# Performance work log

Measured on AMD Instinct MI355X. Metric: run time of the kernel, lower is better.

## Reference

```python
import jax, jax.numpy as jnp
import numpy as np

B, C, H, W = 16, 256, 32, 32
NUM_LAYERS = 30
OUT = 16  # sqrt(out_channels)
EPS = 1e-5


def setup_inputs() -> dict:
    key = jax.random.key(0)
    k1, k2, k3 = jax.random.split(key, 3)
    x = jax.random.normal(k1, (B, C, H, W), dtype=jnp.float32)
    # delta_t ~ small positive values (module inits ~N(0.01, 0.005))
    delta_t = jax.random.uniform(k2, (NUM_LAYERS, 1), dtype=jnp.float32) * 0.02
    matrices = jax.random.normal(k3, (NUM_LAYERS, 1, 1, OUT, OUT), dtype=jnp.float32) * 0.1
    gamma = jnp.ones((H * W,), dtype=jnp.float32)   # BatchNorm2d weight, oc = i*i = H*W
    beta = jnp.zeros((H * W,), dtype=jnp.float32)   # BatchNorm2d bias
    return {"x": x, "delta_t": delta_t, "matrices": matrices, "gamma": gamma, "beta": beta}


def _bn_relu6(z, gamma, beta):
    # training-mode BatchNorm2d over channel axis 1 (channels = H*W), then ReLU6
    mean = jnp.mean(z, axis=(0, 2, 3), keepdims=True)
    var = jnp.mean(jnp.square(z - mean), axis=(0, 2, 3), keepdims=True)  # biased var
    zhat = (z - mean) * jax.lax.rsqrt(var + EPS)
    g = gamma.reshape(1, -1, 1, 1)
    b = beta.reshape(1, -1, 1, 1)
    return jnp.clip(zhat * g + b, 0.0, 6.0)


def reference(x, delta_t, matrices, gamma, beta):
    b, c, h, w = x.shape
    hw = h * w
    # feature_reshape: [B,C,H,W] -> [B,HW,C] -> [B,HW,out,out] (inn == out branch)
    x1 = x.reshape(b, c, hw).transpose(0, 2, 1).reshape(b, hw, OUT, OUT)
    dt = jnp.clip(delta_t, 0.0, 6.0)[:, 0]  # relu6(delta_t), shape [L]

    def step(y0, params):
        m, dtl = params  # m: [1,1,out,out] broadcasts elementwise against x1
        dydt = -y0 + _bn_relu6(y0 + m * x1, gamma, beta)
        return y0 + dtl * dydt, None

    y0, _ = jax.lax.scan(step, x1, (matrices, dt))
    # (y0 + x1): [B, HW, out, out] -> view [B,H,W,out*out] -> permute to [B,out*out,H,W]
    y = (y0 + x1).reshape(b, h, w, OUT * OUT).transpose(0, 3, 1, 2)
    return y
```

## Files before the change

kernel.cpp:

```cpp
#include <hip/hip_runtime.h>

typedef float v2f __attribute__((ext_vector_type(2)));

#define HW      1024
#define NLAYERS 30
#define TPB     256

template <int CTRL, int RMASK>
__device__ __forceinline__ float dpp_add(float x) {
    int t = __builtin_amdgcn_update_dpp(0, __builtin_bit_cast(int, x),
                                        CTRL, RMASK, 0xf, true);
    return x + __builtin_bit_cast(float, t);
}
__device__ __forceinline__ float wave_sum64(float x) {
    x = dpp_add<0x111, 0xf>(x);
    x = dpp_add<0x112, 0xf>(x);
    x = dpp_add<0x114, 0xf>(x);
    x = dpp_add<0x118, 0xf>(x);
    x = dpp_add<0x142, 0xa>(x);
    x = dpp_add<0x143, 0xc>(x);
    return x;
}

__global__ __launch_bounds__(TPB) void ode_fused(const float* __restrict__ x,
                                                 const float* __restrict__ delta_t,
                                                 const float* __restrict__ matrices,
                                                 const float* __restrict__ gamma,
                                                 const float* __restrict__ beta,
                                                 float* __restrict__ out) {
    const int bid = blockIdx.x;
    const int p   = ((bid & 7) << 7) | (bid >> 3);
    const int t   = threadIdx.x;

    __shared__ float smat[(NLAYERS + 1) * 256];
    __shared__ float sdt[NLAYERS];
    __shared__ __align__(16) v2f red[2][4];

#pragma unroll
    for (int i = 0; i < NLAYERS; ++i)
        smat[i * 256 + t] = matrices[i * 256 + t];
    if (t < NLAYERS)
        sdt[t] = __builtin_amdgcn_fmed3f(delta_t[t], 0.0f, 6.0f);

    v2f x1[8], y[8];
#pragma unroll
    for (int k = 0; k < 8; ++k) {
        x1[k].x = x[(size_t)(t + 512 * k) * HW + p];
        x1[k].y = x[(size_t)(t + 512 * k + 256) * HW + p];
        y[k] = x1[k];
    }

    const float gp   = gamma[p];
    const float bp   = beta[p];
    const int   wid  = t >> 6;
    const int   lane = t & 63;

    __syncthreads();
    float m_cur = smat[t];

    for (int l = 0; l < NLAYERS; ++l) {
        const float dtl = sdt[l];
        const v2f m2    = {m_cur, m_cur};
        const v2f dt2   = {dtl, dtl};
        const v2f om2   = {1.0f - dtl, 1.0f - dtl};

        v2f z[8];
        v2f sA = {0.f, 0.f}, sB = {0.f, 0.f};
        v2f qA = {0.f, 0.f}, qB = {0.f, 0.f};
#pragma unroll
        for (int k = 0; k < 8; k += 2) {
            z[k]     = __builtin_elementwise_fma(m2, x1[k], y[k]);
            z[k + 1] = __builtin_elementwise_fma(m2, x1[k + 1], y[k + 1]);
            sA += z[k];
            sB += z[k + 1];
            qA = __builtin_elementwise_fma(z[k], z[k], qA);
            qB = __builtin_elementwise_fma(z[k + 1], z[k + 1], qB);
        }
#pragma unroll
        for (int k = 0; k < 8; ++k) y[k] *= om2;

        const v2f sv = sA + sB;
        const v2f qv = qA + qB;
        float s = wave_sum64(sv.x + sv.y);
        float q = wave_sum64(qv.x + qv.y);

        const int par = l & 1;
        if (lane == 63) { v2f w; w.x = s; w.y = q; red[par][wid] = w; }
        m_cur = smat[(l + 1) * 256 + t];
        __syncthreads();

        const float4 r0 = *(const float4*)&red[par][0];
        const float4 r1 = *(const float4*)&red[par][2];
        const float S  = (r0.x + r0.z) + (r1.x + r1.z);
        const float S2 = (r0.y + r0.w) + (r1.y + r1.w);

        const float mean = S * (1.0f / 4096.0f);
        const float var  = fmaf(-mean, mean, S2 * (1.0f / 4096.0f));
        const float rstd = rsqrtf(var + 1e-5f);
        const float g    = gp * rstd;
        const float bb   = fmaf(-mean, g, bp);
        const v2f g2 = {g, g}, b2 = {bb, bb};
        const v2f z0 = {0.f, 0.f}, s6 = {6.f, 6.f};
#pragma unroll
        for (int k = 0; k < 8; ++k) {
            v2f a = __builtin_elementwise_fma(z[k], g2, b2);
            a = __builtin_elementwise_max(a, z0);
            a = __builtin_elementwise_min(a, s6);
            y[k] = __builtin_elementwise_fma(dt2, a, y[k]);
        }
    }

#pragma unroll
    for (int k = 0; k < 8; ++k) {
        out[(size_t)(t + 512 * k) * HW + p]       = y[k].x + x1[k].x;
        out[(size_t)(t + 512 * k + 256) * HW + p] = y[k].y + x1[k].y;
    }
}

extern "C" void kernel_launch(void* const* d_in, const int* in_sizes, int n_in,
                              void* d_out, int out_size, void* d_ws, size_t ws_size,
                              hipStream_t stream) {
    const float* x        = (const float*)d_in[0];
    const float* delta_t  = (const float*)d_in[1];
    const float* matrices = (const float*)d_in[2];
    const float* gamma    = (const float*)d_in[3];
    const float* beta     = (const float*)d_in[4];
    float* out = (float*)d_out;

    ode_fused<<<dim3(HW), dim3(TPB), 0, stream>>>(x, delta_t, matrices, gamma, beta, out);
}
```

Baseline: 116.0 us.

## Process each BN channel with a single wavefront to eliminate block barriers

```diff
diff --git a/kernel.cpp b/kernel.cpp
--- a/kernel.cpp
+++ b/kernel.cpp
@@ -4,7 +4,7 @@
 
 #define HW      1024
 #define NLAYERS 30
-#define TPB     256
+#define TPB     64
 
 template <int CTRL, int RMASK>
 __device__ __forceinline__ float dpp_add(float x) {
@@ -22,98 +22,98 @@
     return x;
 }
 
-__global__ __launch_bounds__(TPB) void ode_fused(const float* __restrict__ x,
-                                                 const float* __restrict__ delta_t,
-                                                 const float* __restrict__ matrices,
-                                                 const float* __restrict__ gamma,
-                                                 const float* __restrict__ beta,
-                                                 float* __restrict__ out) {
-    const int bid = blockIdx.x;
-    const int p   = ((bid & 7) << 7) | (bid >> 3);
-    const int t   = threadIdx.x;
+__global__ __launch_bounds__(TPB, 1) void ode_wave(
+    const float* __restrict__ x, const float* __restrict__ delta_t,
+    const float* __restrict__ matrices, const float* __restrict__ gamma,
+    const float* __restrict__ beta, float* __restrict__ out) {
 
-    __shared__ float smat[(NLAYERS + 1) * 256];
-    __shared__ float sdt[NLAYERS];
-    __shared__ __align__(16) v2f red[2][4];
+    const int bid  = blockIdx.x;
+    const int p    = ((bid & 7) << 7) | (bid >> 3);
+    const int lane = threadIdx.x;
 
+    v2f x1[4][8], y[4][8], z[4][8];
 #pragma unroll
-    for (int i = 0; i < NLAYERS; ++i)
-        smat[i * 256 + t] = matrices[i * 256 + t];
-    if (t < NLAYERS)
-        sdt[t] = __builtin_amdgcn_fmed3f(delta_t[t], 0.0f, 6.0f);
-
-    v2f x1[8], y[8];
+    for (int j = 0; j < 4; ++j) {
+        const size_t base = (size_t)(lane + 64 * j) * HW + p;
 #pragma unroll
-    for (int k = 0; k < 8; ++k) {
-        x1[k].x = x[(size_t)(t + 512 * k) * HW + p];
-        x1[k].y = x[(size_t)(t + 512 * k + 256) * HW + p];
-        y[k] = x1[k];
+        for (int i = 0; i < 8; ++i) {
+            x1[j][i].x = x[base + (size_t)(2 * i)     * 256 * HW];
+            x1[j][i].y = x[base + (size_t)(2 * i + 1) * 256 * HW];
+            y[j][i] = x1[j][i];
+        }
     }
 
-    const float gp   = gamma[p];
-    const float bp   = beta[p];
-    const int   wid  = t >> 6;
-    const int   lane = t & 63;
+    const float gp = gamma[p];
+    const float bp = beta[p];
 
-    __syncthreads();
-    float m_cur = smat[t];
+    float mn[4];
+#pragma unroll
+    for (int j = 0; j < 4; ++j) mn[j] = matrices[64 * j + lane];
+    float dtn = delta_t[0];
 
-    for (int l = 0; l < NLAYERS; ++l) {
-        const float dtl = sdt[l];
-        const v2f m2    = {m_cur, m_cur};
-        const v2f dt2   = {dtl, dtl};
-        const v2f om2   = {1.0f - dtl, 1.0f - dtl};
+    for (int lay = 0; lay < NLAYERS; ++lay) {
+        const float dt = __builtin_amdgcn_fmed3f(dtn, 0.0f, 6.0f);
+        v2f M[4];
+#pragma unroll
+        for (int j = 0; j < 4; ++j) { M[j].x = mn[j]; M[j].y = mn[j]; }
 
-        v2f z[8];
-        v2f sA = {0.f, 0.f}, sB = {0.f, 0.f};
-        v2f qA = {0.f, 0.f}, qB = {0.f, 0.f};
+        const int nl = (lay < NLAYERS - 1) ? lay + 1 : lay;
 #pragma unroll
-        for (int k = 0; k < 8; k += 2) {
-            z[k]     = __builtin_elementwise_fma(m2, x1[k], y[k]);
-            z[k + 1] = __builtin_elementwise_fma(m2, x1[k + 1], y[k + 1]);
-            sA += z[k];
-            sB += z[k + 1];
-            qA = __builtin_elementwise_fma(z[k], z[k], qA);
-            qB = __builtin_elementwise_fma(z[k + 1], z[k + 1], qB);
+        for (int j = 0; j < 4; ++j) mn[j] = matrices[nl * 256 + 64 * j + lane];
+        dtn = delta_t[nl];
+
+        v2f s[4], q[4];
+#pragma unroll
+        for (int j = 0; j < 4; ++j) {
+            s[j] = (v2f){0.0f, 0.0f};
+            q[j] = (v2f){0.0f, 0.0f};
         }
 #pragma unroll
-        for (int k = 0; k < 8; ++k) y[k] *= om2;
+        for (int j = 0; j < 4; ++j) {
+#pragma unroll
+            for (int i = 0; i < 8; ++i) {
+                const v2f zz = __builtin_elementwise_fma(M[j], x1[j][i], y[j][i]);
+                z[j][i] = zz;
+                s[j] += zz;
+                q[j] = __builtin_elementwise_fma(zz, zz, q[j]);
+            }
+        }
 
-        const v2f sv = sA + sB;
-        const v2f qv = qA + qB;
-        float s = wave_sum64(sv.x + sv.y);
-        float q = wave_sum64(qv.x + qv.y);
-
-        const int par = l & 1;
-        if (lane == 63) { v2f w; w.x = s; w.y = q; red[par][wid] = w; }
-        m_cur = smat[(l + 1) * 256 + t];
-        __syncthreads();
-
-        const float4 r0 = *(const float4*)&red[par][0];
-        const float4 r1 = *(const float4*)&red[par][2];
-        const float S  = (r0.x + r0.z) + (r1.x + r1.z);
-        const float S2 = (r0.y + r0.w) + (r1.y + r1.w);
+        const v2f sv = (s[0] + s[1]) + (s[2] + s[3]);
+        const v2f qv = (q[0] + q[1]) + (q[2] + q[3]);
+        const float ssum = wave_sum64(sv.x + sv.y);
+        const float qsum = wave_sum64(qv.x + qv.y);
+        const float S = __shfl(ssum, 63, 64);
+        const float Q = __shfl(qsum, 63, 64);
 
         const float mean = S * (1.0f / 4096.0f);
-        const float var  = fmaf(-mean, mean, S2 * (1.0f / 4096.0f));
+        const float var  = fmaf(-mean, mean, Q * (1.0f / 4096.0f));
         const float rstd = rsqrtf(var + 1e-5f);
         const float g    = gp * rstd;
         const float bb   = fmaf(-mean, g, bp);
-        const v2f g2 = {g, g}, b2 = {bb, bb};
-        const v2f z0 = {0.f, 0.f}, s6 = {6.f, 6.f};
+        const v2f g2 = {g, g}, b2 = {bb, bb}, dt2 = {dt, dt};
+
 #pragma unroll
-        for (int k = 0; k < 8; ++k) {
-            v2f a = __builtin_elementwise_fma(z[k], g2, b2);
-            a = __builtin_elementwise_max(a, z0);
-            a = __builtin_elementwise_min(a, s6);
-            y[k] = __builtin_elementwise_fma(dt2, a, y[k]);
+        for (int j = 0; j < 4; ++j) {
+#pragma unroll
+            for (int i = 0; i < 8; ++i) {
+                v2f a = __builtin_elementwise_fma(z[j][i], g2, b2);
+                a.x = __builtin_amdgcn_fmed3f(a.x, 0.0f, 6.0f);
+                a.y = __builtin_amdgcn_fmed3f(a.y, 0.0f, 6.0f);
+                const v2f d = a - y[j][i];
+                y[j][i] = __builtin_elementwise_fma(dt2, d, y[j][i]);
+            }
         }
     }
 
 #pragma unroll
-    for (int k = 0; k < 8; ++k) {
-        out[(size_t)(t + 512 * k) * HW + p]       = y[k].x + x1[k].x;
-        out[(size_t)(t + 512 * k + 256) * HW + p] = y[k].y + x1[k].y;
+    for (int j = 0; j < 4; ++j) {
+        const size_t base = (size_t)(lane + 64 * j) * HW + p;
+#pragma unroll
+        for (int i = 0; i < 8; ++i) {
+            out[base + (size_t)(2 * i)     * 256 * HW] = y[j][i].x + x1[j][i].x;
+            out[base + (size_t)(2 * i + 1) * 256 * HW] = y[j][i].y + x1[j][i].y;
+        }
     }
 }
 
@@ -127,5 +127,5 @@
     const float* beta     = (const float*)d_in[4];
     float* out = (float*)d_out;
 
-    ode_fused<<<dim3(HW), dim3(TPB), 0, stream>>>(x, delta_t, matrices, gamma, beta, out);
+    ode_wave<<<dim3(HW), dim3(TPB), 0, stream>>>(x, delta_t, matrices, gamma, beta, out);
 }
```

Measured after the change: 136.7 us. 1.18x slower.

## Transpose input to row-major workspace and run ODE on contiguous rows

Applied to the files above, without the earlier changes.

```diff
diff --git a/kernel.cpp b/kernel.cpp
--- a/kernel.cpp
+++ b/kernel.cpp
@@ -1,10 +1,25 @@
 #include <hip/hip_runtime.h>
 
 typedef float v2f __attribute__((ext_vector_type(2)));
+typedef float v4f __attribute__((ext_vector_type(4)));
 
 #define HW      1024
+#define NROWS   4096
 #define NLAYERS 30
 #define TPB     256
+
+static __device__ __forceinline__ v2f pk_fma(v2f a, v2f b, v2f c) {
+    v2f d; asm("v_pk_fma_f32 %0, %1, %2, %3" : "=v"(d) : "v"(a), "v"(b), "v"(c));
+    return d;
+}
+static __device__ __forceinline__ v2f pk_add(v2f a, v2f b) {
+    v2f d; asm("v_pk_add_f32 %0, %1, %2" : "=v"(d) : "v"(a), "v"(b));
+    return d;
+}
+static __device__ __forceinline__ v2f pk_mul(v2f a, v2f b) {
+    v2f d; asm("v_pk_mul_f32 %0, %1, %2" : "=v"(d) : "v"(a), "v"(b));
+    return d;
+}
 
 template <int CTRL, int RMASK>
 __device__ __forceinline__ float dpp_add(float x) {
@@ -20,6 +35,156 @@
     x = dpp_add<0x142, 0xa>(x);
     x = dpp_add<0x143, 0xc>(x);
     return x;
+}
+
+__global__ __launch_bounds__(TPB) void txp64(const float* __restrict__ src,
+                                             float* __restrict__ dst,
+                                             int M, int N) {
+    __shared__ float tile[64][65];
+    const int n0 = blockIdx.x * 64;
+    const int m0 = blockIdx.y * 64;
+    const int tx = threadIdx.x & 63;
+    const int ty = threadIdx.x >> 6;
+#pragma unroll
+    for (int i = 0; i < 16; ++i) {
+        const int r = ty + 4 * i;
+        tile[r][tx] = src[(size_t)(m0 + r) * N + n0 + tx];
+    }
+    __syncthreads();
+#pragma unroll
+    for (int i = 0; i < 16; ++i) {
+        const int r = ty + 4 * i;
+        dst[(size_t)(n0 + r) * M + m0 + tx] = tile[tx][r];
+    }
+}
+
+__global__ __launch_bounds__(TPB, 4) void ode_row(
+    float* ws, const float* __restrict__ delta_t,
+    const float* __restrict__ matrices, const float* __restrict__ gamma,
+    const float* __restrict__ beta) {
+
+    const int p    = blockIdx.x;
+    const int t    = threadIdx.x;
+    const int wid  = t >> 6;
+    const int lane = t & 63;
+    const int c0   = (4 * t) & 255;
+
+    __shared__ __align__(16) v2f red[2][4];
+
+    float* row = ws + (size_t)p * NROWS;
+
+    v2f x1[8], y[8], z[8];
+#pragma unroll
+    for (int k = 0; k < 4; ++k) {
+        const v4f q4 = *(const v4f*)(row + 4 * t + 1024 * k);
+        x1[2 * k]     = (v2f){q4.x, q4.y};
+        x1[2 * k + 1] = (v2f){q4.z, q4.w};
+        y[2 * k]     = x1[2 * k];
+        y[2 * k + 1] = x1[2 * k + 1];
+    }
+
+    const float gp = gamma[p];
+    const float bp = beta[p];
+
+    {
+        const v4f m4 = *(const v4f*)(matrices + c0);
+        const v2f mA = {m4.x, m4.y}, mB = {m4.z, m4.w};
+        v2f s = {0.f, 0.f}, q = {0.f, 0.f};
+#pragma unroll
+        for (int k = 0; k < 4; ++k) {
+            z[2 * k] = pk_fma(mA, x1[2 * k], y[2 * k]);
+            s = pk_add(s, z[2 * k]);
+            q = pk_fma(z[2 * k], z[2 * k], q);
+            z[2 * k + 1] = pk_fma(mB, x1[2 * k + 1], y[2 * k + 1]);
+            s = pk_add(s, z[2 * k + 1]);
+            q = pk_fma(z[2 * k + 1], z[2 * k + 1], q);
+        }
+        const float ss = wave_sum64(s.x + s.y);
+        const float qq = wave_sum64(q.x + q.y);
+        if (lane == 63) red[0][wid] = (v2f){ss, qq};
+    }
+
+    v4f   m_cur4 = *(const v4f*)(matrices + 256 + c0);
+    float dt_cur = delta_t[0];
+    float dt_nxt = delta_t[1];
+    __syncthreads();
+
+    for (int k = 0; k < NLAYERS - 1; ++k) {
+        const int k2 = (k + 2 < NLAYERS) ? k + 2 : NLAYERS - 1;
+        const v4f   m_nxt4 = *(const v4f*)(matrices + k2 * 256 + c0);
+        const float dt_nn  = delta_t[k2];
+
+        const int par = k & 1;
+        const v4f r0 = *(const v4f*)&red[par][0];
+        const v4f r1 = *(const v4f*)&red[par][2];
+        const float S = (r0.x + r0.z) + (r1.x + r1.z);
+        const float Q = (r0.y + r0.w) + (r1.y + r1.w);
+
+        const float dtk  = __builtin_amdgcn_fmed3f(dt_cur, 0.0f, 6.0f);
+        const float mean = S * (1.0f / 4096.0f);
+        const float var  = fmaf(-mean, mean, Q * (1.0f / 4096.0f));
+        const float rstd = rsqrtf(var + 1e-5f);
+        const float g    = gp * rstd;
+        const float b    = fmaf(-mean, g, bp);
+        const v2f g2 = {g, g}, b2 = {b, b};
+        const v2f dt2 = {dtk, dtk};
+        const v2f om2 = {1.0f - dtk, 1.0f - dtk};
+        const v2f mA = {m_cur4.x, m_cur4.y}, mB = {m_cur4.z, m_cur4.w};
+
+        v2f s = {0.f, 0.f}, q = {0.f, 0.f};
+#pragma unroll
+        for (int j = 0; j < 8; ++j) {
+            v2f a = pk_fma(z[j], g2, b2);
+            a.x = __builtin_amdgcn_fmed3f(a.x, 0.0f, 6.0f);
+            a.y = __builtin_amdgcn_fmed3f(a.y, 0.0f, 6.0f);
+            y[j] = pk_mul(om2, y[j]);
+            y[j] = pk_fma(dt2, a, y[j]);
+            z[j] = pk_fma((j & 1) ? mB : mA, x1[j], y[j]);
+            s = pk_add(s, z[j]);
+            q = pk_fma(z[j], z[j], q);
+        }
+        const float ss = wave_sum64(s.x + s.y);
+        const float qq = wave_sum64(q.x + q.y);
+        if (lane == 63) red[par ^ 1][wid] = (v2f){ss, qq};
+
+        m_cur4 = m_nxt4; dt_cur = dt_nxt; dt_nxt = dt_nn;
+        __syncthreads();
+    }
+
+    {
+        const v4f r0 = *(const v4f*)&red[(NLAYERS - 1) & 1][0];
+        const v4f r1 = *(const v4f*)&red[(NLAYERS - 1) & 1][2];
+        const float S = (r0.x + r0.z) + (r1.x + r1.z);
+        const float Q = (r0.y + r0.w) + (r1.y + r1.w);
+
+        const float dtk  = __builtin_amdgcn_fmed3f(dt_cur, 0.0f, 6.0f);
+        const float mean = S * (1.0f / 4096.0f);
+        const float var  = fmaf(-mean, mean, Q * (1.0f / 4096.0f));
+        const float rstd = rsqrtf(var + 1e-5f);
+        const float g    = gp * rstd;
+        const float b    = fmaf(-mean, g, bp);
+        const v2f g2 = {g, g}, b2 = {b, b};
+        const v2f dt2 = {dtk, dtk};
+        const v2f om2 = {1.0f - dtk, 1.0f - dtk};
+
+#pragma unroll
+        for (int k = 0; k < 4; ++k) {
+            v2f o0, o1;
+#pragma unroll
+            for (int h = 0; h < 2; ++h) {
+                const int j = 2 * k + h;
+                v2f a = pk_fma(z[j], g2, b2);
+                a.x = __builtin_amdgcn_fmed3f(a.x, 0.0f, 6.0f);
+                a.y = __builtin_amdgcn_fmed3f(a.y, 0.0f, 6.0f);
+                v2f yy = pk_mul(om2, y[j]);
+                yy = pk_fma(dt2, a, yy);
+                const v2f o = pk_add(yy, x1[j]);
+                if (h == 0) o0 = o; else o1 = o;
+            }
+            v4f o4; o4.x = o0.x; o4.y = o0.y; o4.z = o1.x; o4.w = o1.y;
+            *(v4f*)(row + 4 * t + 1024 * k) = o4;
+        }
+    }
 }
 
 __global__ __launch_bounds__(TPB) void ode_fused(const float* __restrict__ x,
@@ -127,5 +292,13 @@
     const float* beta     = (const float*)d_in[4];
     float* out = (float*)d_out;
 
-    ode_fused<<<dim3(HW), dim3(TPB), 0, stream>>>(x, delta_t, matrices, gamma, beta, out);
-}
+    const size_t need = (size_t)HW * NROWS * sizeof(float);
+    if (d_ws != nullptr && ws_size >= need) {
+        float* ws = (float*)d_ws;
+        txp64<<<dim3(HW / 64, NROWS / 64), dim3(TPB), 0, stream>>>(x, ws, NROWS, HW);
+        ode_row<<<dim3(HW), dim3(TPB), 0, stream>>>(ws, delta_t, matrices, gamma, beta);
+        txp64<<<dim3(NROWS / 64, HW / 64), dim3(TPB), 0, stream>>>(ws, out, HW, NROWS);
+    } else {
+        ode_fused<<<dim3(HW), dim3(TPB), 0, stream>>>(x, delta_t, matrices, gamma, beta, out);
+    }
+}
```

After: 120.0 us. 3.5% more time.
